# Performance work log

Measured on AMD Instinct MI355X. Metric: run time of the kernel, lower is better.

The kernel has to match this reference:

```python
import jax, jax.numpy as jnp
import numpy as np

DT = 0.01  # continuous-time step for the S4D/Vandermonde reservoir kernel


def setup_inputs() -> dict:
    key = jax.random.key(0)
    ks = jax.random.split(key, 10)
    B, H, L, N = 16, 128, 4096, 64
    u = jax.random.normal(ks[0], (B, H, L), dtype=jnp.float32)
    # stable diagonal SSM: real part of Lambda strictly negative
    lambda_re = -0.5 * jax.random.uniform(ks[1], (H, N), dtype=jnp.float32) - 0.1
    lambda_im = jax.random.normal(ks[2], (H, N), dtype=jnp.float32) * np.pi
    w_re = jax.random.normal(ks[3], (H, N), dtype=jnp.float32) / np.sqrt(N)
    w_im = jax.random.normal(ks[4], (H, N), dtype=jnp.float32) / np.sqrt(N)
    d = jax.random.normal(ks[5], (H,), dtype=jnp.float32)
    mlp_w1 = jax.random.normal(ks[6], (H, H), dtype=jnp.float32) / np.sqrt(H)
    mlp_b1 = jnp.zeros((H,), dtype=jnp.float32)
    mlp_w2 = jax.random.normal(ks[7], (H, H), dtype=jnp.float32) / np.sqrt(H)
    mlp_b2 = jnp.zeros((H,), dtype=jnp.float32)
    return {"u": u, "lambda_re": lambda_re, "lambda_im": lambda_im,
            "w_re": w_re, "w_im": w_im, "d": d,
            "mlp_w1": mlp_w1, "mlp_b1": mlp_b1,
            "mlp_w2": mlp_w2, "mlp_b2": mlp_b2}


def reference(u, lambda_re, lambda_im, w_re, w_im, d,
              mlp_w1, mlp_b1, mlp_w2, mlp_b2):
    B, H, L = u.shape
    Lam = lambda_re + 1j * lambda_im          # (H, N) diagonal state matrix
    W = w_re + 1j * w_im                      # (H, N) merged C*B readout
    ell = jnp.arange(L, dtype=jnp.float32)
    # Vandermonde kernel: K[h, l] = sum_n W[h,n] * exp(dt * Lambda[h,n] * l)
    V = jnp.exp((DT * Lam)[:, :, None] * ell[None, None, :])  # (H, N, L)
    K = jnp.einsum('hn,hnl->hl', W, V)                         # (H, L) complex
    # causal FFT convolution (pad to 2L to avoid circular wrap)
    n = 2 * L
    y = jnp.fft.ifft(jnp.fft.fft(u, n=n, axis=-1) * jnp.fft.fft(K, n=n, axis=-1)[None],
                     n=n, axis=-1)[..., :L]
    y = y + d[None, :, None] * u              # skip / feed-through term
    y = y.real                                # Real() projection
    # 1x1-conv MLP with ReLU (mlp_layers = 2)
    h1 = jax.nn.relu(jnp.einsum('oh,bhl->bol', mlp_w1, y) + mlp_b1[None, :, None])
    y2 = jax.nn.relu(jnp.einsum('oh,bhl->bol', mlp_w2, h1) + mlp_b2[None, :, None])
    return y2
```

## Files before the change

kernel.cpp:

```cpp
#include <hip/hip_runtime.h>
#include <hip/hip_bf16.h>

#define B_ 16
#define H_ 128
#define L_ 4096
#define N_ 64
#define DT_ 0.01f

typedef __bf16 bf16;
typedef __bf16 bf16x8 __attribute__((ext_vector_type(8)));
typedef __bf16 bf16x4 __attribute__((ext_vector_type(4)));
typedef float f32x4 __attribute__((ext_vector_type(4)));

#define USWZ(c, k) ((c) * 64 + (((((k) >> 4) ^ ((c) & 3)) << 4) | ((k) & 15)))
#define SSWZ(c, k) ((c) * 128 + (((((k) >> 4) ^ ((c) & 7)) << 4) | ((k) & 15)))

__global__ __launch_bounds__(512, 4) void k_ssm3(
        const float* __restrict__ u,
        const float* __restrict__ lre, const float* __restrict__ lim,
        const float* __restrict__ wre, const float* __restrict__ wim,
        const float* __restrict__ dv,
        const float* __restrict__ w1, const float* __restrict__ w2,
        bf16* __restrict__ w1b, bf16* __restrict__ w2b,
        bf16* __restrict__ ybf) {
    alignas(16) __shared__ char smem[68352];
    bf16*  Ubf  = (bf16*)smem;
    float* Ctr  = (float*)(smem + 8192);
    bf16*  Sbf  = (bf16*)(smem + 41472);
    bf16*  Tm   = (bf16*)(smem + 57856);
    float* lamS = (float*)(smem + 67072);
    float* taps = (float*)(smem + 68096);

    const int tid  = threadIdx.x;
    const int lane = tid & 63, wv = tid >> 6;
    const int cl   = lane & 15, q = lane >> 4;
    const int bId  = blockIdx.x;
    const int h    = bId & 127;
    const int bg   = bId >> 7;

    if (tid < 64) {
        if (bId < 256) w1b[bId * 64 + tid] = (bf16)w1[bId * 64 + tid];
        else           w2b[(bId - 256) * 64 + tid] = (bf16)w2[(bId - 256) * 64 + tid];
    }
    if (tid < 64) {
        lamS[tid]       = lre[h * 64 + tid] * DT_;
        lamS[64 + tid]  = lim[h * 64 + tid] * DT_;
        lamS[128 + tid] = wre[h * 64 + tid];
        lamS[192 + tid] = wim[h * 64 + tid];
    }
    __syncthreads();

    bf16x8 pA0, pA1;
    {
        const int row = wv * 16 + cl;
        const int n = row & 63;
        const bool isIm = row >= 64;
        const float lr = lamS[n], li = lamS[64 + n];
        #pragma unroll
        for (int jj = 0; jj < 8; ++jj) {
            const float p0 = (float)(63 - (q * 8 + jj));
            const float e0 = __expf(p0 * lr);
            pA0[jj] = (bf16)(isIm ? e0 * __sinf(p0 * li) : e0 * __cosf(p0 * li));
            const float p1 = (float)(63 - (32 + q * 8 + jj));
            const float e1 = __expf(p1 * lr);
            pA1[jj] = (bf16)(isIm ? e1 * __sinf(p1 * li) : e1 * __cosf(p1 * li));
        }
    }
    bf16x8 qA[4];
    {
        const float fd = (float)((wv >> 1) * 16 + cl + 1);
        #pragma unroll
        for (int ks = 0; ks < 4; ++ks) {
            #pragma unroll
            for (int nn = 0; nn < 4; ++nn) {
                const int n = ks * 16 + q * 4 + nn;
                const float lr = lamS[n], li = lamS[64 + n];
                const float wr = lamS[128 + n], wi = lamS[192 + n];
                const float e  = __expf(fd * lr);
                const float cr = e * __cosf(fd * li), ci = e * __sinf(fd * li);
                qA[ks][2 * nn]     = (bf16)(wr * cr - wi * ci);
                qA[ks][2 * nn + 1] = (bf16)(-(wr * ci + wi * cr));
            }
        }
    }
    float a64r, a64i;
    {
        const float lr = lamS[lane], li = lamS[64 + lane];
        const float e = __expf(64.f * lr);
        a64r = e * __cosf(64.f * li);
        a64i = e * __sinf(64.f * li);
    }
    {
        const float lr = lamS[lane], li = lamS[64 + lane];
        const float wr = lamS[128 + lane], wi = lamS[192 + lane];
        #pragma unroll
        for (int i = 0; i < 8; ++i) {
            const int dlt = wv * 8 + i;
            const float fd = (float)dlt;
            const float e = __expf(fd * lr);
            float t = wr * e * __cosf(fd * li) - wi * e * __sinf(fd * li);
            #pragma unroll
            for (int d = 1; d < 64; d <<= 1) t += __shfl_xor(t, d, 64);
            if (lane == 0) taps[dlt] = t;
        }
    }
    __syncthreads();

    {
        const int dlt = tid >> 3, j0 = (tid & 7) << 3;
        const float dh = dv[h];
        bf16x8 t;
        #pragma unroll
        for (int e = 0; e < 8; ++e) {
            const int j = j0 + e;
            float v = (j <= dlt) ? taps[dlt - j] : 0.f;
            if (j == dlt) v += dh;
            t[e] = (bf16)v;
        }
        *(bf16x8*)(&Tm[dlt * 72 + j0]) = t;
    }

    const int mt = wv >> 1, nt0 = (wv & 1) * 2;
    for (int it = 0; it < 4; ++it) {
        const int bh = (bg * 4 + it) * 128 + h;
        const float* __restrict__ up = u + (size_t)bh * L_;

        {
            const int c = tid >> 3, j0 = (tid & 7) << 3;
            const float4* src = (const float4*)(up + c * 64 + j0);
            const float4 f0 = src[0], f1 = src[1];
            bf16x8 t;
            t[0] = (bf16)f0.x; t[1] = (bf16)f0.y; t[2] = (bf16)f0.z; t[3] = (bf16)f0.w;
            t[4] = (bf16)f1.x; t[5] = (bf16)f1.y; t[6] = (bf16)f1.z; t[7] = (bf16)f1.w;
            *(bf16x8*)(&Ubf[USWZ(c, j0)]) = t;
        }
        __syncthreads();

        {
            f32x4 acc[4];
            #pragma unroll
            for (int nt = 0; nt < 4; ++nt) acc[nt] = (f32x4){0.f, 0.f, 0.f, 0.f};
            #pragma unroll
            for (int nt = 0; nt < 4; ++nt) {
                const int c = nt * 16 + cl;
                const bf16x8 b0 = *(const bf16x8*)(&Ubf[USWZ(c, q * 8)]);
                acc[nt] = __builtin_amdgcn_mfma_f32_16x16x32_bf16(pA0, b0, acc[nt], 0, 0, 0);
                const bf16x8 bq = *(const bf16x8*)(&Ubf[USWZ(c, 32 + q * 8)]);
                acc[nt] = __builtin_amdgcn_mfma_f32_16x16x32_bf16(pA1, bq, acc[nt], 0, 0, 0);
            }
            #pragma unroll
            for (int nt = 0; nt < 4; ++nt)
                #pragma unroll
                for (int r = 0; r < 4; ++r)
                    Ctr[(wv * 16 + q * 4 + r) * 65 + nt * 16 + cl] = acc[nt][r];
        }
        __syncthreads();

        if (wv == 0) {
            float sr = 0.f, si = 0.f;
            #pragma unroll 8
            for (int c = 0; c < 64; ++c) {
                bf16* sp = &Sbf[SSWZ(c, 2 * lane)];
                sp[0] = (bf16)sr;
                sp[1] = (bf16)si;
                const float cr = Ctr[lane * 65 + c];
                const float ci = Ctr[(64 + lane) * 65 + c];
                const float nr = fmaf(a64r, sr, fmaf(-a64i, si, cr));
                const float ni = fmaf(a64r, si, fmaf(a64i, sr, ci));
                sr = nr; si = ni;
            }
        }
        __syncthreads();

        {
            f32x4 acc[2];
            acc[0] = (f32x4){0.f, 0.f, 0.f, 0.f};
            acc[1] = (f32x4){0.f, 0.f, 0.f, 0.f};
            #pragma unroll
            for (int ks = 0; ks < 4; ++ks) {
                const int k0 = ks * 32 + q * 8;
                #pragma unroll
                for (int j = 0; j < 2; ++j) {
                    const int c = (nt0 + j) * 16 + cl;
                    const bf16x8 bfr = *(const bf16x8*)(&Sbf[SSWZ(c, k0)]);
                    acc[j] = __builtin_amdgcn_mfma_f32_16x16x32_bf16(qA[ks], bfr, acc[j], 0, 0, 0);
                }
            }
            #pragma unroll
            for (int ks = 0; ks < 2; ++ks) {
                const int k0 = ks * 32 + q * 8;
                const bf16x8 a = *(const bf16x8*)(&Tm[(mt * 16 + cl) * 72 + k0]);
                #pragma unroll
                for (int j = 0; j < 2; ++j) {
                    const int c = (nt0 + j) * 16 + cl;
                    const bf16x8 bfr = *(const bf16x8*)(&Ubf[USWZ(c, k0)]);
                    acc[j] = __builtin_amdgcn_mfma_f32_16x16x32_bf16(a, bfr, acc[j], 0, 0, 0);
                }
            }
            bf16* Yb = (bf16*)Ctr;
            #pragma unroll
            for (int j = 0; j < 2; ++j) {
                const int c = (nt0 + j) * 16 + cl;
                bf16x4 yv;
                #pragma unroll
                for (int r = 0; r < 4; ++r) yv[r] = (bf16)acc[j][r];
                *(bf16x4*)(&Yb[c * 72 + mt * 16 + q * 4]) = yv;
            }
        }
        __syncthreads();

        {
            const bf16* Yb = (const bf16*)Ctr;
            const int c = tid >> 3, s0 = (tid & 7) << 3;
            const bf16x8 v = *(const bf16x8*)(&Yb[c * 72 + s0]);
            *(bf16x8*)(ybf + (size_t)bh * L_ + c * 64 + s0) = v;
        }
        __syncthreads();
    }
}

#define YSTR 136
__global__ __launch_bounds__(256, 4) void k_mlp(
        const bf16* __restrict__ ybf,
        const bf16* __restrict__ w1b, const bf16* __restrict__ w2b,
        const float* __restrict__ b1, const float* __restrict__ b2,
        float* __restrict__ out) {
    __shared__ float Ys[128 * 68];
    __shared__ float B1s[H_], B2s[H_];
    bf16* YT = (bf16*)Ys;

    const int tid = threadIdx.x;
    const int b   = blockIdx.x >> 6;
    const int lt  = blockIdx.x & 63;
    const int l0  = lt * 64;

    if (tid < H_) { B1s[tid] = b1[tid]; B2s[tid] = b2[tid]; }

    {
        const int h  = tid >> 1;
        const int lh = (tid & 1) * 32;
        const bf16x8* src = (const bf16x8*)(ybf + ((size_t)b * H_ + h) * L_ + l0 + lh);
        #pragma unroll
        for (int v = 0; v < 4; ++v) {
            bf16x8 d = src[v];
            #pragma unroll
            for (int e = 0; e < 8; ++e) YT[(lh + v * 8 + e) * YSTR + h] = d[e];
        }
    }
    __syncthreads();

    const int lane = tid & 63;
    const int wv   = tid >> 6;
    const int m    = lane & 15;
    const int q    = lane >> 4;
    const int m0   = wv * 32;

    f32x4 acc[2][4];
    #pragma unroll
    for (int i = 0; i < 2; ++i)
        #pragma unroll
        for (int nt = 0; nt < 4; ++nt) acc[i][nt] = (f32x4){0.f, 0.f, 0.f, 0.f};

    #pragma unroll
    for (int kb = 0; kb < 4; ++kb) {
        const bf16x8 a0 = *(const bf16x8*)(w1b + (size_t)(m0 + m)      * H_ + kb * 32 + q * 8);
        const bf16x8 a1 = *(const bf16x8*)(w1b + (size_t)(m0 + 16 + m) * H_ + kb * 32 + q * 8);
        #pragma unroll
        for (int nt = 0; nt < 4; ++nt) {
            const bf16x8 bfr = *(const bf16x8*)(&YT[(nt * 16 + m) * YSTR + kb * 32 + q * 8]);
            acc[0][nt] = __builtin_amdgcn_mfma_f32_16x16x32_bf16(a0, bfr, acc[0][nt], 0, 0, 0);
            acc[1][nt] = __builtin_amdgcn_mfma_f32_16x16x32_bf16(a1, bfr, acc[1][nt], 0, 0, 0);
        }
    }
    __syncthreads();

    #pragma unroll
    for (int i = 0; i < 2; ++i) {
        const int o0 = m0 + 16 * i + 4 * q;
        #pragma unroll
        for (int nt = 0; nt < 4; ++nt) {
            const f32x4 v = acc[i][nt];
            bf16x4 hv;
            #pragma unroll
            for (int r = 0; r < 4; ++r) {
                float x = v[r] + B1s[o0 + r];
                hv[r] = (bf16)fmaxf(x, 0.f);
            }
            *(bf16x4*)(&YT[(nt * 16 + m) * YSTR + o0]) = hv;
        }
    }
    __syncthreads();

    f32x4 acc2[2][4];
    #pragma unroll
    for (int i = 0; i < 2; ++i)
        #pragma unroll
        for (int nt = 0; nt < 4; ++nt) acc2[i][nt] = (f32x4){0.f, 0.f, 0.f, 0.f};

    #pragma unroll
    for (int kb = 0; kb < 4; ++kb) {
        const bf16x8 a0 = *(const bf16x8*)(w2b + (size_t)(m0 + m)      * H_ + kb * 32 + q * 8);
        const bf16x8 a1 = *(const bf16x8*)(w2b + (size_t)(m0 + 16 + m) * H_ + kb * 32 + q * 8);
        #pragma unroll
        for (int nt = 0; nt < 4; ++nt) {
            const bf16x8 bfr = *(const bf16x8*)(&YT[(nt * 16 + m) * YSTR + kb * 32 + q * 8]);
            acc2[0][nt] = __builtin_amdgcn_mfma_f32_16x16x32_bf16(a0, bfr, acc2[0][nt], 0, 0, 0);
            acc2[1][nt] = __builtin_amdgcn_mfma_f32_16x16x32_bf16(a1, bfr, acc2[1][nt], 0, 0, 0);
        }
    }
    __syncthreads();

    #pragma unroll
    for (int i = 0; i < 2; ++i) {
        const int o0 = m0 + 16 * i + 4 * q;
        #pragma unroll
        for (int nt = 0; nt < 4; ++nt) {
            const f32x4 v = acc2[i][nt];
            #pragma unroll
            for (int r = 0; r < 4; ++r) {
                float x = v[r] + B2s[o0 + r];
                Ys[(o0 + r) * 68 + nt * 16 + m] = fmaxf(x, 0.f);
            }
        }
    }
    __syncthreads();

    {
        const int rg = tid >> 4, c4 = (tid & 15) << 2;
        float* op = out + ((size_t)b * H_) * L_ + l0;
        #pragma unroll
        for (int v = 0; v < 8; ++v) {
            const int row = v * 16 + rg;
            const float4 val = *(const float4*)(&Ys[row * 68 + c4]);
            *(float4*)(op + (size_t)row * L_ + c4) = val;
        }
    }
}

extern "C" void kernel_launch(void* const* d_in, const int* in_sizes, int n_in,
                              void* d_out, int out_size, void* d_ws, size_t ws_size,
                              hipStream_t stream) {
    const float* u   = (const float*)d_in[0];
    const float* lre = (const float*)d_in[1];
    const float* lim = (const float*)d_in[2];
    const float* wre = (const float*)d_in[3];
    const float* wim = (const float*)d_in[4];
    const float* dv  = (const float*)d_in[5];
    const float* w1  = (const float*)d_in[6];
    const float* b1  = (const float*)d_in[7];
    const float* w2  = (const float*)d_in[8];
    const float* b2  = (const float*)d_in[9];
    float* out = (float*)d_out;

    char* ws = (char*)d_ws;
    bf16* ybf = (bf16*)ws;   ws += (size_t)B_ * H_ * L_ * 2;
    bf16* w1b = (bf16*)ws;   ws += H_ * H_ * 2;
    bf16* w2b = (bf16*)ws;   ws += H_ * H_ * 2;

    hipLaunchKernelGGL(k_ssm3, dim3(512), dim3(512), 0, stream,
                       u, lre, lim, wre, wim, dv, w1, w2, w1b, w2b, ybf);
    hipLaunchKernelGGL(k_mlp, dim3(B_ * (L_ / 64)), dim3(256), 0, stream,
                       ybf, w1b, w2b, b1, b2, out);
}
```

Measured before the change: 131.2 us.

## Overlap serial scan with local MFMA term and shrink MLP shared memory

In the SSM kernel, waves 1-7 now compute the intra-chunk Toeplitz MFMA contribution while wave 0 runs the serial chunk-state scan. Wave 0 does its share after the barrier, so that work is no longer serialized behind the scan. In the MLP kernel, the fp32 shared staging buffer for the output is dropped and results are written straight to global memory from the MFMA layout. This shrinks LDS enough to raise the occupancy hint from 4 to 6 blocks, at the cost of less coalesced 16-wide global stores.

```diff
diff --git a/kernel.cpp b/kernel.cpp
--- a/kernel.cpp
+++ b/kernel.cpp
@@ -156,6 +156,9 @@
         }
         __syncthreads();
 
+        f32x4 acc2[2];
+        acc2[0] = (f32x4){0.f, 0.f, 0.f, 0.f};
+        acc2[1] = (f32x4){0.f, 0.f, 0.f, 0.f};
         if (wv == 0) {
             float sr = 0.f, si = 0.f;
             #pragma unroll 8
@@ -169,13 +172,35 @@
                 const float ni = fmaf(a64r, si, fmaf(a64i, sr, ci));
                 sr = nr; si = ni;
             }
-        }
-        __syncthreads();
-
+        } else {
+            #pragma unroll
+            for (int ks = 0; ks < 2; ++ks) {
+                const int k0 = ks * 32 + q * 8;
+                const bf16x8 a = *(const bf16x8*)(&Tm[(mt * 16 + cl) * 72 + k0]);
+                #pragma unroll
+                for (int j = 0; j < 2; ++j) {
+                    const int c = (nt0 + j) * 16 + cl;
+                    const bf16x8 bfr = *(const bf16x8*)(&Ubf[USWZ(c, k0)]);
+                    acc2[j] = __builtin_amdgcn_mfma_f32_16x16x32_bf16(a, bfr, acc2[j], 0, 0, 0);
+                }
+            }
+        }
+        __syncthreads();
+
+        if (wv == 0) {
+            #pragma unroll
+            for (int ks = 0; ks < 2; ++ks) {
+                const int k0 = ks * 32 + q * 8;
+                const bf16x8 a = *(const bf16x8*)(&Tm[(mt * 16 + cl) * 72 + k0]);
+                #pragma unroll
+                for (int j = 0; j < 2; ++j) {
+                    const int c = (nt0 + j) * 16 + cl;
+                    const bf16x8 bfr = *(const bf16x8*)(&Ubf[USWZ(c, k0)]);
+                    acc2[j] = __builtin_amdgcn_mfma_f32_16x16x32_bf16(a, bfr, acc2[j], 0, 0, 0);
+                }
+            }
+        }
         {
-            f32x4 acc[2];
-            acc[0] = (f32x4){0.f, 0.f, 0.f, 0.f};
-            acc[1] = (f32x4){0.f, 0.f, 0.f, 0.f};
             #pragma unroll
             for (int ks = 0; ks < 4; ++ks) {
                 const int k0 = ks * 32 + q * 8;
@@ -183,18 +208,7 @@
                 for (int j = 0; j < 2; ++j) {
                     const int c = (nt0 + j) * 16 + cl;
                     const bf16x8 bfr = *(const bf16x8*)(&Sbf[SSWZ(c, k0)]);
-                    acc[j] = __builtin_amdgcn_mfma_f32_16x16x32_bf16(qA[ks], bfr, acc[j], 0, 0, 0);
-                }
-            }
-            #pragma unroll
-            for (int ks = 0; ks < 2; ++ks) {
-                const int k0 = ks * 32 + q * 8;
-                const bf16x8 a = *(const bf16x8*)(&Tm[(mt * 16 + cl) * 72 + k0]);
-                #pragma unroll
-                for (int j = 0; j < 2; ++j) {
-                    const int c = (nt0 + j) * 16 + cl;
-                    const bf16x8 bfr = *(const bf16x8*)(&Ubf[USWZ(c, k0)]);
-                    acc[j] = __builtin_amdgcn_mfma_f32_16x16x32_bf16(a, bfr, acc[j], 0, 0, 0);
+                    acc2[j] = __builtin_amdgcn_mfma_f32_16x16x32_bf16(qA[ks], bfr, acc2[j], 0, 0, 0);
                 }
             }
             bf16* Yb = (bf16*)Ctr;
@@ -203,7 +217,7 @@
                 const int c = (nt0 + j) * 16 + cl;
                 bf16x4 yv;
                 #pragma unroll
-                for (int r = 0; r < 4; ++r) yv[r] = (bf16)acc[j][r];
+                for (int r = 0; r < 4; ++r) yv[r] = (bf16)acc2[j][r];
                 *(bf16x4*)(&Yb[c * 72 + mt * 16 + q * 4]) = yv;
             }
         }
@@ -220,14 +234,13 @@
 }
 
 #define YSTR 136
-__global__ __launch_bounds__(256, 4) void k_mlp(
+__global__ __launch_bounds__(256, 6) void k_mlp(
         const bf16* __restrict__ ybf,
         const bf16* __restrict__ w1b, const bf16* __restrict__ w2b,
         const float* __restrict__ b1, const float* __restrict__ b2,
         float* __restrict__ out) {
-    __shared__ float Ys[128 * 68];
+    __shared__ bf16 YT[64 * YSTR];
     __shared__ float B1s[H_], B2s[H_];
-    bf16* YT = (bf16*)Ys;
 
     const int tid = threadIdx.x;
     const int b   = blockIdx.x >> 6;
@@ -308,7 +321,6 @@
             acc2[1][nt] = __builtin_amdgcn_mfma_f32_16x16x32_bf16(a1, bfr, acc2[1][nt], 0, 0, 0);
         }
     }
-    __syncthreads();
 
     #pragma unroll
     for (int i = 0; i < 2; ++i) {
@@ -319,20 +331,9 @@
             #pragma unroll
             for (int r = 0; r < 4; ++r) {
                 float x = v[r] + B2s[o0 + r];
-                Ys[(o0 + r) * 68 + nt * 16 + m] = fmaxf(x, 0.f);
-            }
-        }
-    }
-    __syncthreads();
-
-    {
-        const int rg = tid >> 4, c4 = (tid & 15) << 2;
-        float* op = out + ((size_t)b * H_) * L_ + l0;
-        #pragma unroll
-        for (int v = 0; v < 8; ++v) {
-            const int row = v * 16 + rg;
-            const float4 val = *(const float4*)(&Ys[row * 68 + c4]);
-            *(float4*)(op + (size_t)row * L_ + c4) = val;
+                x = fmaxf(x, 0.f);
+                out[((size_t)b * H_ + o0 + r) * L_ + l0 + nt * 16 + m] = x;
+            }
         }
     }
 }
```

Result: no change. 129.2 us (-1.5%).
